# Performance work log

Measured on AMD Instinct MI355X. Metric: run time of the kernel, lower is better.

The kernel has to match this reference:

```python
import jax, jax.numpy as jnp
import numpy as np

DIM = 512
HEADS = 16
DIM_HEAD = 64
INNER = HEADS * DIM_HEAD
MAX_T = 32
BASE = 10000.0


def rotate_half(t):
    t1, t2 = jnp.split(t, 2, axis=-1)
    return jnp.concatenate((-t2, t1), axis=-1)


def setup_inputs() -> dict:
    key = jax.random.key(0)
    ks = jax.random.split(key, 12)
    B, T, S = 2, 16, 128
    x = jax.random.normal(ks[0], (B, T, S, DIM), dtype=jnp.float32)
    y = jax.random.normal(ks[1], (B, T, S, DIM), dtype=jnp.float32)
    temporal_mask = jax.random.randint(ks[2], (B, T, T), 0, 2).astype(jnp.int32)
    sc = 1.0 / np.sqrt(DIM)
    Wq = jax.random.normal(ks[3], (DIM, INNER), dtype=jnp.float32) * sc
    Wk = jax.random.normal(ks[4], (DIM, INNER), dtype=jnp.float32) * sc
    Wv = jax.random.normal(ks[5], (DIM, INNER), dtype=jnp.float32) * sc
    Wo = jax.random.normal(ks[6], (INNER, DIM), dtype=jnp.float32) / np.sqrt(INNER)
    bo = jnp.zeros((DIM,), dtype=jnp.float32)
    pos_emb = jax.random.normal(ks[7], (MAX_T, DIM), dtype=jnp.float32)
    gate_w = jax.random.normal(ks[8], (DIM, 1), dtype=jnp.float32) * sc
    gate_b = jnp.zeros((1,), dtype=jnp.float32)
    return {"x": x, "y": y, "temporal_mask": temporal_mask, "Wq": Wq, "Wk": Wk,
            "Wv": Wv, "Wo": Wo, "bo": bo, "pos_emb": pos_emb,
            "gate_w": gate_w, "gate_b": gate_b}


def reference(x, y, temporal_mask, Wq, Wk, Wv, Wo, bo, pos_emb, gate_w, gate_b):
    B, T, S, D = x.shape
    n = T * S
    scale = DIM_HEAD ** (-0.5)
    # temporal positional embedding (T <= MAX_T path)
    tp = pos_emb[:T][None, :, None, :]  # [1,T,1,D]
    x = x + tp
    y = y + tp
    xf = x.reshape(B, n, D)
    yf = y.reshape(B, n, D)
    # NOTE: k is computed from x (as in the source), v from y
    q = (xf @ Wq).reshape(B, n, HEADS, DIM_HEAD).transpose(0, 2, 1, 3)
    k = (xf @ Wk).reshape(B, n, HEADS, DIM_HEAD).transpose(0, 2, 1, 3)
    v = (yf @ Wv).reshape(B, n, HEADS, DIM_HEAD).transpose(0, 2, 1, 3)
    # RoPE over flattened token index
    inv_freq = 1.0 / (BASE ** (jnp.arange(0, DIM_HEAD, 2, dtype=jnp.float32) / DIM_HEAD))
    freqs = jnp.arange(n, dtype=jnp.float32)[:, None] * inv_freq[None, :]  # [n, d/2]
    emb = jnp.concatenate((freqs, freqs), axis=-1)  # [n, d]
    fc = jnp.cos(emb)[None, None, :, :]
    fs = jnp.sin(emb)[None, None, :, :]
    q = q * fc + rotate_half(q) * fs
    k = k * fc + rotate_half(k) * fs
    dots = jnp.einsum('bhid,bhjd->bhij', q, k) * scale  # [B,H,n,n]
    # expand temporal mask [B,T,T] -> [B,1,n,n] block structure
    m = jnp.repeat(jnp.repeat(temporal_mask, S, axis=1), S, axis=2)[:, None, :, :]
    dots = jnp.where(m == 0, -jnp.inf, dots)
    attn = jax.nn.softmax(dots, axis=-1)
    out = jnp.einsum('bhij,bhjd->bhid', attn, v)  # [B,H,n,d]
    out = out.transpose(0, 2, 1, 3).reshape(B, n, INNER)
    out = out @ Wo + bo
    out = out.reshape(B, T, S, D)
    gate = jax.nn.sigmoid(out @ gate_w + gate_b)  # [B,T,S,1]
    return out * gate
```

## Files before the change

kernel.cpp:

```cpp
#include <hip/hip_runtime.h>
#include <hip/hip_bf16.h>

typedef __attribute__((ext_vector_type(4))) short short4v;
typedef __attribute__((ext_vector_type(8))) short short8v;
typedef __attribute__((ext_vector_type(4))) float float4v;
typedef __attribute__((ext_vector_type(2))) unsigned int uint2v;
typedef __attribute__((ext_vector_type(4))) unsigned int uint4v;

#define NTOK 2048
#define MROWS 4096
#define DMODEL 512
#define NINNER 1024
#define DH 64
#define HH 16
#define LOG2E 1.4426950408889634f

__device__ __forceinline__ unsigned short b2s(float f) {
    __hip_bfloat16 h = __float2bfloat16(f);
    return __builtin_bit_cast(unsigned short, h);
}
__device__ __forceinline__ float bf2f(unsigned short h) {
    unsigned int u = ((unsigned int)h) << 16;
    return __builtin_bit_cast(float, u);
}

__device__ __forceinline__ float4v mfma32(short8v a, short8v b, float4v c) {
    return __builtin_amdgcn_mfma_f32_16x16x32_bf16(a, b, c, 0, 0, 0);
}

__device__ __forceinline__ void gld16(const void* g, void* l) {
    __builtin_amdgcn_global_load_lds((const __attribute__((address_space(1))) void*)g,
                                     (__attribute__((address_space(3))) void*)l, 16, 0, 0);
}

__global__ void k_pre(const float* __restrict__ x, const float* __restrict__ y,
                      const float* __restrict__ pe,
                      unsigned short* __restrict__ xpb, unsigned short* __restrict__ ypb,
                      const float* __restrict__ Wq, const float* __restrict__ Wk,
                      const float* __restrict__ Wv, const float* __restrict__ Wo,
                      unsigned short* __restrict__ wall, unsigned short* __restrict__ wot,
                      float* __restrict__ ctab, float* __restrict__ stab) {
    int blk = blockIdx.x;
    if (blk < 2048) {
        int e0 = (blk * 256 + threadIdx.x) * 4;
        int row = e0 >> 9, col = e0 & 511;
        int t = (row & (NTOK - 1)) >> 7;
        const float4v xv = *(const float4v*)(x + e0);
        const float4v yv = *(const float4v*)(y + e0);
        const float4v pv = *(const float4v*)(pe + t * DMODEL + col);
        short4v xo, yo;
#pragma unroll
        for (int i = 0; i < 4; ++i) {
            xo[i] = (short)b2s(xv[i] + pv[i]);
            yo[i] = (short)b2s(yv[i] + pv[i]);
        }
        *(short4v*)(xpb + e0) = xo;
        *(short4v*)(ypb + e0) = yo;
    } else if (blk < 8192) {
        int which = (blk - 2048) >> 11;
        int idx = ((blk - 2048) & 2047) * 256 + threadIdx.x;
        const float* W = (which == 0) ? Wq : (which == 1) ? Wk : Wv;
        int n = idx & 1023, k = idx >> 10;
        wall[(which * 1024 + n) * 512 + k] = b2s(W[idx]);
    } else if (blk < 10240) {
        int idx = (blk - 8192) * 256 + threadIdx.x;
        int n = idx & 511, k = idx >> 9;
        wot[n * 1024 + k] = b2s(Wo[idx]);
    } else {
        int idx = (blk - 10240) * 256 + threadIdx.x;
        int p = idx >> 5, j = idx & 31;
        float invf = powf(10000.0f, -(float)(2 * j) * (1.0f / 64.0f));
        float f = (float)p * invf;
        ctab[idx] = cosf(f);
        stab[idx] = sinf(f);
    }
}

__global__ __launch_bounds__(256) void k_qkv(const unsigned short* __restrict__ A,
                                             const unsigned short* __restrict__ A2,
                                             const unsigned short* __restrict__ Bt,
                                             unsigned short* __restrict__ Cq,
                                             unsigned short* __restrict__ Ck,
                                             unsigned short* __restrict__ Cvv,
                                             const float* __restrict__ ctab,
                                             const float* __restrict__ stab,
                                             float scale) {
    __shared__ unsigned short Ab[2][4096];
    __shared__ unsigned short Bb[2][4096];
    const int tid = threadIdx.x;
    const int w = tid >> 6, l = tid & 63, l16 = l & 15, g = l >> 4;
    const int wm = w >> 1, wn = w & 1;
    const int m0 = blockIdx.y * 128, n0 = blockIdx.x * 128;
    const unsigned short* Ap = (n0 >= 2048) ? A2 : A;
    float4v acc[4][4];
#pragma unroll
    for (int i = 0; i < 4; ++i)
#pragma unroll
        for (int j = 0; j < 4; ++j) acc[i][j] = (float4v){0.f, 0.f, 0.f, 0.f};

    auto stage = [&](int t, int buf) {
        int k0 = t * 32;
#pragma unroll
        for (int it = 0; it < 2; ++it) {
            int f = it * 4 + w;
            gld16(Ap + (size_t)(m0 + f * 16 + l16) * 512 + k0 + g * 8, &Ab[buf][f * 512]);
            gld16(Bt + (size_t)(n0 + f * 16 + l16) * 512 + k0 + g * 8, &Bb[buf][f * 512]);
        }
    };

    stage(0, 0);
    __syncthreads();
    for (int t = 0; t < 16; ++t) {
        const int cur = t & 1;
        if (t + 1 < 16) stage(t + 1, cur ^ 1);
        short8v af[4], bf[4];
#pragma unroll
        for (int mi = 0; mi < 4; ++mi)
            af[mi] = *(const short8v*)&Ab[cur][(wm * 4 + mi) * 512 + l * 8];
#pragma unroll
        for (int nj = 0; nj < 4; ++nj)
            bf[nj] = *(const short8v*)&Bb[cur][(wn * 4 + nj) * 512 + l * 8];
        __builtin_amdgcn_s_setprio(1);
#pragma unroll
        for (int mi = 0; mi < 4; ++mi)
#pragma unroll
            for (int nj = 0; nj < 4; ++nj)
                acc[mi][nj] = mfma32(af[mi], bf[nj], acc[mi][nj]);
        __builtin_amdgcn_s_setprio(0);
        __syncthreads();
    }

    const int hh = (n0 + wn * 64) >> 6;
    const int head = hh & 15;
    if (hh < 32) {
        unsigned short* out = (hh < 16) ? Cq : Ck;
        const float sc = (hh < 16) ? scale : 1.0f;
#pragma unroll
        for (int mi = 0; mi < 4; ++mi)
#pragma unroll
            for (int r = 0; r < 4; ++r) {
                int row = m0 + wm * 64 + mi * 16 + g * 4 + r;
                int b = row >> 11, pos = row & (NTOK - 1);
                const float* cr = ctab + pos * 32;
                const float* sr = stab + pos * 32;
                unsigned short* ob = out + (size_t)((b * HH + head) * NTOK + pos) * DH;
#pragma unroll
                for (int nj = 0; nj < 2; ++nj) {
                    int j = nj * 16 + l16;
                    float c = cr[j], s = sr[j];
                    float v1 = acc[mi][nj][r], v2 = acc[mi][nj + 2][r];
                    ob[j] = b2s((v1 * c - v2 * s) * sc);
                    ob[j + 32] = b2s((v2 * c + v1 * s) * sc);
                }
            }
    } else {
#pragma unroll
        for (int mi = 0; mi < 4; ++mi)
#pragma unroll
            for (int nj = 0; nj < 4; ++nj) {
                int d = nj * 16 + l16;
                int row0 = m0 + wm * 64 + mi * 16 + g * 4;
                int b = row0 >> 11, pos0 = row0 & (NTOK - 1);
                short4v o;
#pragma unroll
                for (int r = 0; r < 4; ++r) o[r] = (short)b2s(acc[mi][nj][r]);
                *(short4v*)(Cvv + (size_t)((b * HH + head) * DH + d) * NTOK + pos0) = o;
            }
    }
}

__global__ __launch_bounds__(256) void k_gemm0(const unsigned short* __restrict__ A,
                                               const unsigned short* __restrict__ Bt,
                                               float* __restrict__ C,
                                               const float* __restrict__ bias,
                                               int M, int N, int K) {
    __shared__ unsigned short Ab[2][4096];
    __shared__ unsigned short Bb[2][2048];
    const int tid = threadIdx.x;
    const int w = tid >> 6, l = tid & 63, l16 = l & 15, g = l >> 4;
    const int m0 = blockIdx.y * 128, n0 = blockIdx.x * 64;
    float4v acc[2][4];
#pragma unroll
    for (int i = 0; i < 2; ++i)
#pragma unroll
        for (int j = 0; j < 4; ++j) acc[i][j] = (float4v){0.f, 0.f, 0.f, 0.f};

    const int nstep = K >> 5;
    auto stage = [&](int t, int buf) {
        int k0 = t * 32;
#pragma unroll
        for (int s = 0; s < 2; ++s) {
            int fi = s * 4 + w;
            gld16(A + (size_t)(m0 + fi * 16 + l16) * K + k0 + g * 8, &Ab[buf][fi * 512]);
        }
        gld16(Bt + (size_t)(n0 + w * 16 + l16) * K + k0 + g * 8, &Bb[buf][w * 512]);
    };

    stage(0, 0);
    __syncthreads();
    for (int t = 0; t < nstep; ++t) {
        const int cur = t & 1;
        if (t + 1 < nstep) stage(t + 1, cur ^ 1);
        short8v af[2], bf[4];
#pragma unroll
        for (int mi = 0; mi < 2; ++mi)
            af[mi] = *(const short8v*)&Ab[cur][(w * 2 + mi) * 512 + l * 8];
#pragma unroll
        for (int nj = 0; nj < 4; ++nj)
            bf[nj] = *(const short8v*)&Bb[cur][nj * 512 + l * 8];
        __builtin_amdgcn_s_setprio(1);
#pragma unroll
        for (int mi = 0; mi < 2; ++mi)
#pragma unroll
            for (int nj = 0; nj < 4; ++nj)
                acc[mi][nj] = mfma32(af[mi], bf[nj], acc[mi][nj]);
        __builtin_amdgcn_s_setprio(0);
        __syncthreads();
    }
#pragma unroll
    for (int mi = 0; mi < 2; ++mi)
#pragma unroll
        for (int nj = 0; nj < 4; ++nj) {
            int col = n0 + nj * 16 + l16;
            float bv = bias[col];
#pragma unroll
            for (int r = 0; r < 4; ++r) {
                int row = m0 + w * 32 + mi * 16 + g * 4 + r;
                C[(size_t)row * N + col] = acc[mi][nj][r] + bv;
            }
        }
}

__global__ __launch_bounds__(512, 4) void k_attn(const unsigned short* __restrict__ qh,
                                                 const unsigned short* __restrict__ kh,
                                                 const unsigned short* __restrict__ vt,
                                                 const int* __restrict__ tmask,
                                                 unsigned short* __restrict__ otmp) {
    __shared__ unsigned short Kb[2][8192];
    __shared__ unsigned short Vb[8192];
    __shared__ int tlist[17];
    const int blk = blockIdx.x;
    const int u = (blk & 7) * 64 + (blk >> 3);
    const int ti = u & 15, h = (u >> 4) & 15, b = u >> 8;
    const int tid = threadIdx.x, w = tid >> 6, l = tid & 63, l16 = l & 15, g = l >> 4;
    if (tid == 0) {
        int c = 0;
        for (int j = 0; j < 16; ++j)
            if (tmask[(b * 16 + ti) * 16 + j]) tlist[c++] = j;
        tlist[16] = c;
    }
    __syncthreads();
    const int cnt = tlist[16];
    const unsigned short* qb = qh + (size_t)((b * HH + h) * NTOK) * DH;
    const unsigned short* kb = kh + (size_t)((b * HH + h) * NTOK) * DH;
    const unsigned short* vb = vt + (size_t)((b * HH + h) * DH) * NTOK;
    const int q0 = ti * 128 + w * 16;

    short8v qf[2];
#pragma unroll
    for (int c = 0; c < 2; ++c)
        qf[c] = *(const short8v*)(qb + (size_t)(q0 + l16) * DH + c * 32 + g * 8);

    float4v oacc[4];
#pragma unroll
    for (int i = 0; i < 4; ++i) oacc[i] = (float4v){0.f, 0.f, 0.f, 0.f};
    float mx = -1e30f, lrow = 0.f;
    uint4v vrg[2];

    auto stageK = [&](int tj, int buf) {
#pragma unroll
        for (int s = 0; s < 2; ++s) {
            int fi = w * 2 + s;
            const unsigned short* ga =
                kb + (size_t)(tj * 128 + (fi >> 1) * 16 + l16) * DH + (fi & 1) * 32 + g * 8;
            gld16(ga, &Kb[buf][fi * 512]);
        }
    };
    auto loadV = [&](int tj) {
#pragma unroll
        for (int s = 0; s < 2; ++s) {
            int fi = w * 2 + s;
            const unsigned short* ga =
                vb + (size_t)((fi >> 2) * 16 + l16) * NTOK + tj * 128 + (fi & 3) * 32 + g * 4;
            uint2v lo = *(const uint2v*)ga;
            uint2v hi = *(const uint2v*)(ga + 16);
            vrg[s] = (uint4v){lo[0], lo[1], hi[0], hi[1]};
        }
    };
    auto writeV = [&]() {
#pragma unroll
        for (int s = 0; s < 2; ++s)
            *(uint4v*)&Vb[(w * 2 + s) * 512 + l * 8] = vrg[s];
    };

    if (cnt > 0) {
        stageK(tlist[0], 0);
        loadV(tlist[0]);
        writeV();
        __syncthreads();
        for (int i = 0; i < cnt; ++i) {
            const int cur = i & 1;
            const bool pre = (i + 1 < cnt);
            if (pre) { stageK(tlist[i + 1], cur ^ 1); loadV(tlist[i + 1]); }
            float4v sacc[8];
#pragma unroll
            for (int jk = 0; jk < 8; ++jk) sacc[jk] = (float4v){0.f, 0.f, 0.f, 0.f};
            __builtin_amdgcn_s_setprio(1);
#pragma unroll
            for (int jk = 0; jk < 8; ++jk) {
                short8v kf0 = *(const short8v*)&Kb[cur][(jk * 2 + 0) * 512 + l * 8];
                short8v kf1 = *(const short8v*)&Kb[cur][(jk * 2 + 1) * 512 + l * 8];
                sacc[jk] = mfma32(kf0, qf[0], sacc[jk]);
                sacc[jk] = mfma32(kf1, qf[1], sacc[jk]);
            }
            __builtin_amdgcn_s_setprio(0);
            float tm = -1e30f;
#pragma unroll
            for (int jk = 0; jk < 8; ++jk) {
                float4v s4 = sacc[jk];
                tm = fmaxf(tm, fmaxf(fmaxf(s4[0], s4[1]), fmaxf(s4[2], s4[3])));
            }
            tm = fmaxf(tm, __shfl_xor(tm, 16));
            tm = fmaxf(tm, __shfl_xor(tm, 32));
            if (!__all(tm <= mx + 8.0f)) {
                float mnew = fmaxf(mx, tm);
                float alpha = exp2f(mx - mnew);
                lrow *= alpha;
#pragma unroll
                for (int md = 0; md < 4; ++md)
#pragma unroll
                    for (int r = 0; r < 4; ++r) oacc[md][r] *= alpha;
                mx = mnew;
            }
            short8v pf[4];
            float4v tsv = {0.f, 0.f, 0.f, 0.f};
#pragma unroll
            for (int cc = 0; cc < 4; ++cc) {
                float p[8];
#pragma unroll
                for (int r = 0; r < 4; ++r) {
                    p[r] = exp2f(sacc[2 * cc][r] - mx);
                    p[r + 4] = exp2f(sacc[2 * cc + 1][r] - mx);
                }
                short8v pv;
#pragma unroll
                for (int r = 0; r < 4; ++r) {
                    tsv[r] += p[r] + p[r + 4];
                    pv[r] = (short)b2s(p[r]);
                    pv[r + 4] = (short)b2s(p[r + 4]);
                }
                pf[cc] = pv;
            }
            float ts = (tsv[0] + tsv[1]) + (tsv[2] + tsv[3]);
            ts += __shfl_xor(ts, 16);
            ts += __shfl_xor(ts, 32);
            lrow += ts;
            __builtin_amdgcn_s_setprio(1);
#pragma unroll
            for (int md = 0; md < 4; ++md)
#pragma unroll
                for (int cc = 0; cc < 4; ++cc) {
                    short8v vf = *(const short8v*)&Vb[(md * 4 + cc) * 512 + l * 8];
                    oacc[md] = mfma32(vf, pf[cc], oacc[md]);
                }
            __builtin_amdgcn_s_setprio(0);
            __syncthreads();
            if (pre) writeV();
            __syncthreads();
        }
    }
    float inv = lrow > 0.f ? 1.0f / lrow : 0.f;
    int q = q0 + l16;
#pragma unroll
    for (int md = 0; md < 4; ++md) {
        short4v o;
#pragma unroll
        for (int r = 0; r < 4; ++r) o[r] = (short)b2s(oacc[md][r] * inv);
        *(short4v*)(otmp + (size_t)(b * NTOK + q) * NINNER + h * DH + md * 16 + g * 4) = o;
    }
}

__global__ __launch_bounds__(256) void k_gate(const float* __restrict__ proj,
                                              const float* __restrict__ gw,
                                              const float* __restrict__ gb,
                                              float* __restrict__ out) {
    int row = blockIdx.x * 4 + (threadIdx.x >> 6);
    int l = threadIdx.x & 63;
    const float* pr = proj + (size_t)row * DMODEL;
    float acc = 0.f;
#pragma unroll
    for (int c = 0; c < DMODEL; c += 64) acc += pr[c + l] * gw[c + l];
#pragma unroll
    for (int off = 32; off > 0; off >>= 1) acc += __shfl_xor(acc, off);
    float gt = 1.0f / (1.0f + __expf(-(acc + gb[0])));
    float* orow = out + (size_t)row * DMODEL;
#pragma unroll
    for (int c = 0; c < DMODEL; c += 64) orow[c + l] = pr[c + l] * gt;
}

extern "C" void kernel_launch(void* const* d_in, const int* in_sizes, int n_in,
                              void* d_out, int out_size, void* d_ws, size_t ws_size,
                              hipStream_t stream) {
    (void)in_sizes; (void)n_in; (void)out_size; (void)ws_size;
    const float* x = (const float*)d_in[0];
    const float* y = (const float*)d_in[1];
    const int* tmask = (const int*)d_in[2];
    const float* Wq = (const float*)d_in[3];
    const float* Wk = (const float*)d_in[4];
    const float* Wv = (const float*)d_in[5];
    const float* Wo = (const float*)d_in[6];
    const float* bo = (const float*)d_in[7];
    const float* pe = (const float*)d_in[8];
    const float* gw = (const float*)d_in[9];
    const float* gb = (const float*)d_in[10];

    char* ws = (char*)d_ws;
    const size_t MB = 1u << 20;
    unsigned short* xpb  = (unsigned short*)(ws + 0);
    unsigned short* ypb  = (unsigned short*)(ws + 4 * MB);
    unsigned short* wall = (unsigned short*)(ws + 8 * MB);
    unsigned short* wot  = (unsigned short*)(ws + 11 * MB);
    unsigned short* qh   = (unsigned short*)(ws + 12 * MB);
    unsigned short* kh   = (unsigned short*)(ws + 20 * MB);
    unsigned short* vt   = (unsigned short*)(ws + 28 * MB);
    unsigned short* otm  = (unsigned short*)(ws + 36 * MB);
    float* proj = (float*)(ws + 44 * MB);
    float* ct = (float*)(ws + 52 * MB);
    float* st = (float*)(ws + 52 * MB + 256 * 1024);
    float* outp = (float*)d_out;

    k_pre<<<10496, 256, 0, stream>>>(x, y, pe, xpb, ypb, Wq, Wk, Wv, Wo,
                                     wall, wot, ct, st);
    k_qkv<<<dim3(24, 32), 256, 0, stream>>>(xpb, ypb, wall, qh, kh, vt, ct, st,
                                            0.125f * LOG2E);
    k_attn<<<512, 512, 0, stream>>>(qh, kh, vt, tmask, otm);
    k_gemm0<<<dim3(8, 32), 256, 0, stream>>>(otm, wot, proj, bo, 4096, 512, 1024);
    k_gate<<<1024, 256, 0, stream>>>(proj, gw, gb, outp);
}
```

Baseline: 134.8 us.

## Fuse gate into output projection, tile weight transposes, double-buffer V in attention

```diff
diff --git a/kernel.cpp b/kernel.cpp
--- a/kernel.cpp
+++ b/kernel.cpp
@@ -38,11 +38,16 @@
                       unsigned short* __restrict__ xpb, unsigned short* __restrict__ ypb,
                       const float* __restrict__ Wq, const float* __restrict__ Wk,
                       const float* __restrict__ Wv, const float* __restrict__ Wo,
+                      const float* __restrict__ gwv, const float* __restrict__ gbv,
+                      const float* __restrict__ bo,
                       unsigned short* __restrict__ wall, unsigned short* __restrict__ wot,
-                      float* __restrict__ ctab, float* __restrict__ stab) {
-    int blk = blockIdx.x;
+                      float* __restrict__ ctab, float* __restrict__ stab,
+                      unsigned short* __restrict__ gvp, float* __restrict__ bgp) {
+    __shared__ float tl[64][65];
+    const int blk = blockIdx.x;
+    const int tid = threadIdx.x;
     if (blk < 2048) {
-        int e0 = (blk * 256 + threadIdx.x) * 4;
+        int e0 = (blk * 256 + tid) * 4;
         int row = e0 >> 9, col = e0 & 511;
         int t = (row & (NTOK - 1)) >> 7;
         const float4v xv = *(const float4v*)(x + e0);
@@ -56,23 +61,67 @@
         }
         *(short4v*)(xpb + e0) = xo;
         *(short4v*)(ypb + e0) = yo;
-    } else if (blk < 8192) {
-        int which = (blk - 2048) >> 11;
-        int idx = ((blk - 2048) & 2047) * 256 + threadIdx.x;
-        const float* W = (which == 0) ? Wq : (which == 1) ? Wk : Wv;
-        int n = idx & 1023, k = idx >> 10;
-        wall[(which * 1024 + n) * 512 + k] = b2s(W[idx]);
-    } else if (blk < 10240) {
-        int idx = (blk - 8192) * 256 + threadIdx.x;
-        int n = idx & 511, k = idx >> 9;
-        wot[n * 1024 + k] = b2s(Wo[idx]);
-    } else {
-        int idx = (blk - 10240) * 256 + threadIdx.x;
+    } else if (blk < 2560) {
+        int t = blk - 2048;
+        const float* W;
+        unsigned short* dst;
+        int K, N, k0, n0;
+        if (t < 384) {
+            int which = t / 128, tile = t % 128;
+            W = (which == 0) ? Wq : (which == 1) ? Wk : Wv;
+            dst = wall + (size_t)which * 1024 * 512;
+            K = 512; N = 1024;
+            k0 = (tile >> 4) * 64; n0 = (tile & 15) * 64;
+        } else {
+            int tile = t - 384;
+            W = Wo; dst = wot;
+            K = 1024; N = 512;
+            k0 = (tile >> 3) * 64; n0 = (tile & 7) * 64;
+        }
+        int tx = tid & 63, ty4 = tid >> 6;
+#pragma unroll
+        for (int p = 0; p < 16; ++p) {
+            int ky = p * 4 + ty4;
+            tl[ky][tx] = W[(size_t)(k0 + ky) * N + n0 + tx];
+        }
+        __syncthreads();
+#pragma unroll
+        for (int p = 0; p < 16; ++p) {
+            int ny = p * 4 + ty4;
+            dst[(size_t)(n0 + ny) * K + k0 + tx] = b2s(tl[tx][ny]);
+        }
+    } else if (blk < 2816) {
+        int idx = (blk - 2560) * 256 + tid;
         int p = idx >> 5, j = idx & 31;
         float invf = powf(10000.0f, -(float)(2 * j) * (1.0f / 64.0f));
         float f = (float)p * invf;
         ctab[idx] = cosf(f);
         stab[idx] = sinf(f);
+    } else if (blk < 2832) {
+        int base = (blk - 2816) * 64;
+        int w = tid >> 6, l = tid & 63, l16 = l & 15, g = l >> 4;
+        int row = base + w * 16 + l16;
+        const float* wr = Wo + (size_t)row * 512 + g * 128;
+        const float* gr = gwv + g * 128;
+        float s = 0.f;
+#pragma unroll
+        for (int t = 0; t < 32; ++t) {
+            float4v a = *(const float4v*)(wr + t * 4);
+            float4v b = *(const float4v*)(gr + t * 4);
+            s += a[0] * b[0] + a[1] * b[1] + a[2] * b[2] + a[3] * b[3];
+        }
+        s += __shfl_xor(s, 16);
+        s += __shfl_xor(s, 32);
+        if (g == 0) gvp[row] = b2s(s);
+    } else {
+        if (tid < 64) {
+            float s = 0.f;
+#pragma unroll
+            for (int t = 0; t < 8; ++t) s += bo[tid + t * 64] * gwv[tid + t * 64];
+#pragma unroll
+            for (int off = 32; off > 0; off >>= 1) s += __shfl_xor(s, off);
+            if (tid == 0) bgp[0] = s + gbv[0];
+        }
     }
 }
 
@@ -169,13 +218,15 @@
     }
 }
 
-__global__ __launch_bounds__(256) void k_gemm0(const unsigned short* __restrict__ A,
+__global__ __launch_bounds__(256) void k_oproj(const unsigned short* __restrict__ A,
                                                const unsigned short* __restrict__ Bt,
-                                               float* __restrict__ C,
-                                               const float* __restrict__ bias,
-                                               int M, int N, int K) {
+                                               const float* __restrict__ bo,
+                                               const unsigned short* __restrict__ gv,
+                                               const float* __restrict__ bgp,
+                                               float* __restrict__ out) {
     __shared__ unsigned short Ab[2][4096];
     __shared__ unsigned short Bb[2][2048];
+    __shared__ float glds[128];
     const int tid = threadIdx.x;
     const int w = tid >> 6, l = tid & 63, l16 = l & 15, g = l >> 4;
     const int m0 = blockIdx.y * 128, n0 = blockIdx.x * 64;
@@ -184,23 +235,23 @@
     for (int i = 0; i < 2; ++i)
 #pragma unroll
         for (int j = 0; j < 4; ++j) acc[i][j] = (float4v){0.f, 0.f, 0.f, 0.f};
-
-    const int nstep = K >> 5;
+    float gp0 = 0.f, gp1 = 0.f;
+
     auto stage = [&](int t, int buf) {
         int k0 = t * 32;
 #pragma unroll
         for (int s = 0; s < 2; ++s) {
             int fi = s * 4 + w;
-            gld16(A + (size_t)(m0 + fi * 16 + l16) * K + k0 + g * 8, &Ab[buf][fi * 512]);
-        }
-        gld16(Bt + (size_t)(n0 + w * 16 + l16) * K + k0 + g * 8, &Bb[buf][w * 512]);
+            gld16(A + (size_t)(m0 + fi * 16 + l16) * 1024 + k0 + g * 8, &Ab[buf][fi * 512]);
+        }
+        gld16(Bt + (size_t)(n0 + w * 16 + l16) * 1024 + k0 + g * 8, &Bb[buf][w * 512]);
     };
 
     stage(0, 0);
     __syncthreads();
-    for (int t = 0; t < nstep; ++t) {
+    for (int t = 0; t < 32; ++t) {
         const int cur = t & 1;
-        if (t + 1 < nstep) stage(t + 1, cur ^ 1);
+        if (t + 1 < 32) stage(t + 1, cur ^ 1);
         short8v af[2], bf[4];
 #pragma unroll
         for (int mi = 0; mi < 2; ++mi)
@@ -208,6 +259,7 @@
 #pragma unroll
         for (int nj = 0; nj < 4; ++nj)
             bf[nj] = *(const short8v*)&Bb[cur][nj * 512 + l * 8];
+        short8v gvv = *(const short8v*)(gv + t * 32 + g * 8);
         __builtin_amdgcn_s_setprio(1);
 #pragma unroll
         for (int mi = 0; mi < 2; ++mi)
@@ -215,29 +267,44 @@
             for (int nj = 0; nj < 4; ++nj)
                 acc[mi][nj] = mfma32(af[mi], bf[nj], acc[mi][nj]);
         __builtin_amdgcn_s_setprio(0);
+#pragma unroll
+        for (int j = 0; j < 8; ++j) {
+            float gf = bf2f((unsigned short)gvv[j]);
+            gp0 = fmaf(bf2f((unsigned short)af[0][j]), gf, gp0);
+            gp1 = fmaf(bf2f((unsigned short)af[1][j]), gf, gp1);
+        }
         __syncthreads();
     }
+    gp0 += __shfl_xor(gp0, 16); gp0 += __shfl_xor(gp0, 32);
+    gp1 += __shfl_xor(gp1, 16); gp1 += __shfl_xor(gp1, 32);
+    const float bg = bgp[0];
+    if (g == 0) {
+        glds[w * 32 + l16] = 1.0f / (1.0f + __expf(-(gp0 + bg)));
+        glds[w * 32 + 16 + l16] = 1.0f / (1.0f + __expf(-(gp1 + bg)));
+    }
+    __syncthreads();
 #pragma unroll
     for (int mi = 0; mi < 2; ++mi)
 #pragma unroll
         for (int nj = 0; nj < 4; ++nj) {
             int col = n0 + nj * 16 + l16;
-            float bv = bias[col];
+            float bv = bo[col];
 #pragma unroll
             for (int r = 0; r < 4; ++r) {
                 int row = m0 + w * 32 + mi * 16 + g * 4 + r;
-                C[(size_t)row * N + col] = acc[mi][nj][r] + bv;
-            }
-        }
-}
-
-__global__ __launch_bounds__(512, 4) void k_attn(const unsigned short* __restrict__ qh,
-                                                 const unsigned short* __restrict__ kh,
-                                                 const unsigned short* __restrict__ vt,
-                                                 const int* __restrict__ tmask,
-                                                 unsigned short* __restrict__ otmp) {
+                float gt = glds[w * 32 + mi * 16 + g * 4 + r];
+                out[(size_t)row * 512 + col] = (acc[mi][nj][r] + bv) * gt;
+            }
+        }
+}
+
+__global__ __launch_bounds__(512) void k_attn(const unsigned short* __restrict__ qh,
+                                              const unsigned short* __restrict__ kh,
+                                              const unsigned short* __restrict__ vt,
+                                              const int* __restrict__ tmask,
+                                              unsigned short* __restrict__ otmp) {
     __shared__ unsigned short Kb[2][8192];
-    __shared__ unsigned short Vb[8192];
+    __shared__ unsigned short Vb[2][8192];
     __shared__ int tlist[17];
     const int blk = blockIdx.x;
     const int u = (blk & 7) * 64 + (blk >> 3);
@@ -287,16 +354,16 @@
             vrg[s] = (uint4v){lo[0], lo[1], hi[0], hi[1]};
         }
     };
-    auto writeV = [&]() {
+    auto writeV = [&](int buf) {
 #pragma unroll
         for (int s = 0; s < 2; ++s)
-            *(uint4v*)&Vb[(w * 2 + s) * 512 + l * 8] = vrg[s];
+            *(uint4v*)&Vb[buf][(w * 2 + s) * 512 + l * 8] = vrg[s];
     };
 
     if (cnt > 0) {
         stageK(tlist[0], 0);
         loadV(tlist[0]);
-        writeV();
+        writeV(0);
         __syncthreads();
         for (int i = 0; i < cnt; ++i) {
             const int cur = i & 1;
@@ -355,18 +422,17 @@
             ts += __shfl_xor(ts, 16);
             ts += __shfl_xor(ts, 32);
             lrow += ts;
+            if (pre) writeV(cur ^ 1);
             __builtin_amdgcn_s_setprio(1);
 #pragma unroll
             for (int md = 0; md < 4; ++md)
 #pragma unroll
                 for (int cc = 0; cc < 4; ++cc) {
-                    short8v vf = *(const short8v*)&Vb[(md * 4 + cc) * 512 + l * 8];
+                    short8v vf = *(const short8v*)&Vb[cur][(md * 4 + cc) * 512 + l * 8];
                     oacc[md] = mfma32(vf, pf[cc], oacc[md]);
                 }
             __builtin_amdgcn_s_setprio(0);
             __syncthreads();
-            if (pre) writeV();
-            __syncthreads();
         }
     }
     float inv = lrow > 0.f ? 1.0f / lrow : 0.f;
@@ -378,24 +444,6 @@
         for (int r = 0; r < 4; ++r) o[r] = (short)b2s(oacc[md][r] * inv);
         *(short4v*)(otmp + (size_t)(b * NTOK + q) * NINNER + h * DH + md * 16 + g * 4) = o;
     }
-}
-
-__global__ __launch_bounds__(256) void k_gate(const float* __restrict__ proj,
-                                              const float* __restrict__ gw,
-                                              const float* __restrict__ gb,
-                                              float* __restrict__ out) {
-    int row = blockIdx.x * 4 + (threadIdx.x >> 6);
-    int l = threadIdx.x & 63;
-    const float* pr = proj + (size_t)row * DMODEL;
-    float acc = 0.f;
-#pragma unroll
-    for (int c = 0; c < DMODEL; c += 64) acc += pr[c + l] * gw[c + l];
-#pragma unroll
-    for (int off = 32; off > 0; off >>= 1) acc += __shfl_xor(acc, off);
-    float gt = 1.0f / (1.0f + __expf(-(acc + gb[0])));
-    float* orow = out + (size_t)row * DMODEL;
-#pragma unroll
-    for (int c = 0; c < DMODEL; c += 64) orow[c + l] = pr[c + l] * gt;
 }
 
 extern "C" void kernel_launch(void* const* d_in, const int* in_sizes, int n_in,
@@ -424,16 +472,16 @@
     unsigned short* kh   = (unsigned short*)(ws + 20 * MB);
     unsigned short* vt   = (unsigned short*)(ws + 28 * MB);
     unsigned short* otm  = (unsigned short*)(ws + 36 * MB);
-    float* proj = (float*)(ws + 44 * MB);
-    float* ct = (float*)(ws + 52 * MB);
-    float* st = (float*)(ws + 52 * MB + 256 * 1024);
+    float* ct = (float*)(ws + 44 * MB);
+    float* st = (float*)(ws + 44 * MB + 256 * 1024);
+    unsigned short* gv = (unsigned short*)(ws + 45 * MB);
+    float* bg = (float*)(ws + 45 * MB + 4096);
     float* outp = (float*)d_out;
 
-    k_pre<<<10496, 256, 0, stream>>>(x, y, pe, xpb, ypb, Wq, Wk, Wv, Wo,
-                                     wall, wot, ct, st);
+    k_pre<<<2833, 256, 0, stream>>>(x, y, pe, xpb, ypb, Wq, Wk, Wv, Wo, gw, gb, bo,
+                                    wall, wot, ct, st, gv, bg);
     k_qkv<<<dim3(24, 32), 256, 0, stream>>>(xpb, ypb, wall, qh, kh, vt, ct, st,
                                             0.125f * LOG2E);
     k_attn<<<512, 512, 0, stream>>>(qh, kh, vt, tmask, otm);
-    k_gemm0<<<dim3(8, 32), 256, 0, stream>>>(otm, wot, proj, bo, 4096, 512, 1024);
-    k_gate<<<1024, 256, 0, stream>>>(proj, gw, gb, outp);
-}
+    k_oproj<<<dim3(8, 32), 256, 0, stream>>>(otm, wot, bo, gv, bg, outp);
+}
```

Result: no change. 135.6 us (+0.6%).
